# Optimization experiments

Measured on AMD Instinct MI355X. Metric: run time of the kernel, lower is better.

## Reference

```python
import jax, jax.numpy as jnp
import numpy as np

N_NODES = 50000
N_EDGES = 800000
F_IN = 32
F_OUT = 32
NB = 4  # basis terms per dimension


def linear_basis(x, n):
    # Piecewise-linear 'hat' basis on [-1, 1] with n equispaced centers.
    # f_k(x) = max(0, 1 - |x - c_k| / dx),  c_k = linspace(-1, 1, n), dx = 2/(n-1)
    centers = jnp.linspace(-1.0, 1.0, n, dtype=x.dtype)
    dx = 2.0 / (n - 1)
    return jnp.maximum(0.0, 1.0 - jnp.abs(x[:, None] - centers) / dx)  # [E, n]


def setup_inputs() -> dict:
    key = jax.random.key(0)
    k0, k1, k2, k3, k4 = jax.random.split(key, 5)
    x_i = jax.random.normal(k0, (N_NODES, F_IN), dtype=jnp.float32)
    x_j = jax.random.normal(k1, (N_NODES, F_IN), dtype=jnp.float32)
    edge_index = jax.random.randint(k2, (2, N_EDGES), 0, N_NODES)  # row0=target, row1=source
    edge_attr = jax.random.uniform(k3, (N_EDGES, 2), dtype=jnp.float32,
                                   minval=-1.0, maxval=1.0)
    # torch init: uniform_(-0.05, 0.05) on [NB, NB, F_IN, F_OUT]
    weight = jax.random.uniform(k4, (NB, NB, F_IN, F_OUT), dtype=jnp.float32,
                                minval=-0.05, maxval=0.05)
    return {"x_i": x_i, "x_j": x_j, "edge_index": edge_index,
            "edge_attr": edge_attr, "weight": weight}


def reference(x_i, x_j, edge_index, edge_attr, weight):
    dst = edge_index[0]  # aggregation target nodes
    src = edge_index[1]  # source nodes (features gathered from x_j)

    bx = linear_basis(edge_attr[:, 0], NB)            # [E, NB]
    by = linear_basis(edge_attr[:, 1], NB)            # [E, NB]
    b = (bx[:, :, None] * by[:, None, :]).reshape(-1, NB * NB)  # [E, NB*NB]

    feat = x_j[src]                                   # [E, F_IN] edge gather
    w = weight.reshape(NB * NB, F_IN, F_OUT)          # [K, F_IN, F_OUT]
    msg = jnp.einsum('ek,ei,kio->eo', b, feat, w)     # [E, F_OUT]

    # weighted scatter-add to target nodes
    out = jax.ops.segment_sum(msg, dst, num_segments=x_i.shape[0])  # [N, F_OUT]
    return out
```

## Files before the change

kernel.cpp:

```cpp
#include <hip/hip_runtime.h>
#include <hip/hip_bf16.h>

typedef short short8 __attribute__((ext_vector_type(8)));
typedef float f32x4 __attribute__((ext_vector_type(4)));
typedef unsigned uint4v __attribute__((ext_vector_type(4)));

#define F 32
#define NB 4
#define BINSH 5
#define BINSZ 32
#define EPB 512
#define SCH 4096
#define MAXBIN 2048
#define CAPB 2048
#define OSCH 2048
#define OMAXNBLK 1024

__device__ __forceinline__ short f2bf(float f) {
    unsigned u = __float_as_uint(f);
    unsigned r = (u + 0x7FFFu + ((u >> 16) & 1u)) >> 16;
    return (short)r;
}

__device__ __forceinline__ unsigned pk2(float a, float b) {
    __hip_bfloat162 h = __float22bfloat162_rn(make_float2(a, b));
    union { __hip_bfloat162 h; unsigned u; } cv; cv.h = h; return cv.u;
}

__global__ __launch_bounds__(256) void w_prep(
    const float* __restrict__ w, short* __restrict__ wbf)
{
    int idx = blockIdx.x * 256 + threadIdx.x;
    int k = idx >> 10, rem = idx & 1023, i = rem >> 5, o = rem & 31;
    int slot = (((k * 4 + (i >> 3)) * 2 + (o >> 4)) * 16 + (o & 15)) * 8 + (i & 7);
    wbf[slot] = f2bf(w[idx]);
}

__global__ __launch_bounds__(256) void h2_kernel(
    const int* __restrict__ ei, const float* __restrict__ attr, int E, int nbin,
    int* __restrict__ bincnt, int* __restrict__ cellcnt)
{
    __shared__ int hb[MAXBIN];
    __shared__ int hc[9];
    int t = threadIdx.x;
    for (int i = t; i < nbin; i += 256) hb[i] = 0;
    if (t < 9) hc[t] = 0;
    __syncthreads();
    int stride = gridDim.x * blockDim.x;
    for (int e = blockIdx.x * blockDim.x + t; e < E; e += stride) {
        int dst = ei[e];
        float2 a = reinterpret_cast<const float2*>(attr)[e];
        float tx = fminf(fmaxf((a.x + 1.0f) * 1.5f, 0.f), 3.f);
        float ty = fminf(fmaxf((a.y + 1.0f) * 1.5f, 0.f), 3.f);
        int kx = min((int)tx, 2), ky = min((int)ty, 2);
        atomicAdd(&hb[dst >> BINSH], 1);
        atomicAdd(&hc[kx * 3 + ky], 1);
    }
    __syncthreads();
    for (int i = t; i < nbin; i += 256)
        if (hb[i]) atomicAdd(&bincnt[i], hb[i]);
    if (t < 9 && hc[t]) atomicAdd(&cellcnt[t], hc[t]);
}

__global__ __launch_bounds__(256) void scan2_kernel(
    const int* __restrict__ bincnt, int* __restrict__ binbase,
    int* __restrict__ bincur, const int* __restrict__ cellcnt,
    int* __restrict__ cellbase, int* __restrict__ cellcur,
    int* __restrict__ blkoff, int nbin)
{
    __shared__ int part[256];
    int t = threadIdx.x;
    int chunk = (nbin + 255) / 256;
    int lo = t * chunk, hi = min(lo + chunk, nbin);
    int s = 0;
    for (int q = lo; q < hi; ++q) s += bincnt[q];
    part[t] = s;
    __syncthreads();
    if (t == 0) {
        int run = 0;
        for (int j = 0; j < 256; ++j) { int v = part[j]; part[j] = run; run += v; }
        binbase[nbin] = run;
    }
    __syncthreads();
    int run = part[t];
    for (int q = lo; q < hi; ++q) {
        binbase[q] = run; bincur[q] = run;
        run += bincnt[q];
    }
    if (t == 0) {
        int off = 0, boff = 0;
        for (int c = 0; c < 9; ++c) {
            cellbase[c] = off; cellcur[c] = off; blkoff[c] = boff;
            off  += cellcnt[c];
            boff += (cellcnt[c] + EPB - 1) / EPB;
        }
        cellbase[9] = off; blkoff[9] = boff;
    }
}

__global__ __launch_bounds__(256) void scat2_kernel(
    const int* __restrict__ ei, const float* __restrict__ attr, int E, int nbin,
    int* __restrict__ bincur, int* __restrict__ cellcur,
    uint4* __restrict__ cellrec, unsigned char* __restrict__ dloc8)
{
    __shared__ int hb[MAXBIN];
    __shared__ int hc[9];
    int t = threadIdx.x, b = blockIdx.x;
    int start = b * SCH, end = min(start + SCH, E);
    for (int i = t; i < nbin; i += 256) hb[i] = 0;
    if (t < 9) hc[t] = 0;
    __syncthreads();
    for (int e = start + t; e < end; e += 256) {
        int dst = ei[e];
        float2 a = reinterpret_cast<const float2*>(attr)[e];
        float tx = fminf(fmaxf((a.x + 1.0f) * 1.5f, 0.f), 3.f);
        float ty = fminf(fmaxf((a.y + 1.0f) * 1.5f, 0.f), 3.f);
        int kx = min((int)tx, 2), ky = min((int)ty, 2);
        atomicAdd(&hb[dst >> BINSH], 1);
        atomicAdd(&hc[kx * 3 + ky], 1);
    }
    __syncthreads();
    for (int k = t; k < nbin; k += 256) {
        int c = hb[k];
        if (c) hb[k] = atomicAdd(&bincur[k], c);
    }
    if (t < 9) hc[t] = atomicAdd(&cellcur[t], hc[t]);
    __syncthreads();
    for (int e = start + t; e < end; e += 256) {
        int dst = ei[e];
        int src = ei[E + e];
        float2 a = reinterpret_cast<const float2*>(attr)[e];
        float tx = fminf(fmaxf((a.x + 1.0f) * 1.5f, 0.f), 3.f);
        float ty = fminf(fmaxf((a.y + 1.0f) * 1.5f, 0.f), 3.f);
        int kx = min((int)tx, 2), ky = min((int)ty, 2);
        int pd = atomicAdd(&hb[dst >> BINSH], 1);
        int pc = atomicAdd(&hc[kx * 3 + ky], 1);
        uint4 rec;
        rec.x = (unsigned)src;
        rec.y = (unsigned)pd;
        rec.z = __float_as_uint(tx);
        rec.w = __float_as_uint(ty);
        cellrec[pc] = rec;
        dloc8[pd] = (unsigned char)(dst & (BINSZ - 1));
    }
}

__global__ __launch_bounds__(256, 4) void bconv_msg(
    const float* __restrict__ x_j, const short* __restrict__ wbf,
    const int* __restrict__ cellbase, const int* __restrict__ blkoff,
    const uint4* __restrict__ cellrec, unsigned* __restrict__ msg)
{
    int b = blockIdx.x;
    if (b >= blkoff[9]) return;
    int c = 0;
    #pragma unroll
    for (int q = 1; q < 9; ++q) c += (b >= blkoff[q]) ? 1 : 0;
    int kx0 = c / 3, ky0 = c - 3 * (c / 3);
    int local  = b - blkoff[c];
    int cstart = cellbase[c], cend = cellbase[c + 1];
    int pstart = cstart + local * EPB;
    int pend   = min(pstart + EPB, cend);
    if (pstart >= pend) return;

    int t = threadIdx.x;
    int wid = t >> 6, lane = t & 63;
    int row16 = lane & 15, hi = lane >> 4;

    short8 w0[4], w1[4];
    #pragma unroll
    for (int kk = 0; kk < 4; ++kk) {
        int ks = (kx0 + (kk >> 1)) * NB + (ky0 + (kk & 1));
        w0[kk] = *reinterpret_cast<const short8*>(
            wbf + (((ks * 4 + hi) * 2 + 0) * 16 + row16) * 8);
        w1[kk] = *reinterpret_cast<const short8*>(
            wbf + (((ks * 4 + hi) * 2 + 1) * 16 + row16) * 8);
    }

    const float4* x4 = reinterpret_cast<const float4*>(x_j);
    int ntile = (pend - pstart + 15) >> 4;

    auto fetch = [&](int ti, uint4& rec, float4& fa, float4& fb, int& pdv) {
        int p = pstart + ti * 16 + row16;
        bool v = p < pend;
        int pp = v ? p : pstart;
        rec = cellrec[pp];
        int src = rec.x;
        fa = x4[src * 8 + 2 * hi];
        fb = x4[src * 8 + 2 * hi + 1];
        pdv = v ? (int)rec.y : -1;
    };

    int it = wid;
    uint4 rec; float4 fa, fb; int pdv;
    if (it < ntile) fetch(it, rec, fa, fb, pdv);

    for (; it < ntile; it += 4) {
        uint4 recN; float4 faN, fbN; int pdvN = -1;
        bool hn = (it + 4) < ntile;
        if (hn) fetch(it + 4, recN, faN, fbN, pdvN);

        float tx = __uint_as_float(rec.z), ty = __uint_as_float(rec.w);
        float fx = tx - (float)kx0, fy = ty - (float)ky0;
        float bx0 = 1.f - fx, by0 = 1.f - fy;
        float bc[4] = { bx0 * by0, bx0 * fy, fx * by0, fx * fy };
        float fl[8] = { fa.x, fa.y, fa.z, fa.w, fb.x, fb.y, fb.z, fb.w };

        f32x4 a0 = {0,0,0,0}, a1 = {0,0,0,0};
        #pragma unroll
        for (int kk = 0; kk < 4; ++kk) {
            float s = bc[kk];
            uint4v u;
            u[0] = pk2(fl[0] * s, fl[1] * s);
            u[1] = pk2(fl[2] * s, fl[3] * s);
            u[2] = pk2(fl[4] * s, fl[5] * s);
            u[3] = pk2(fl[6] * s, fl[7] * s);
            short8 av = __builtin_bit_cast(short8, u);
            a0 = __builtin_amdgcn_mfma_f32_16x16x32_bf16(av, w0[kk], a0, 0, 0, 0);
            a1 = __builtin_amdgcn_mfma_f32_16x16x32_bf16(av, w1[kk], a1, 0, 0, 0);
        }
        #pragma unroll
        for (int r = 0; r < 4; ++r) {
            int pd = __shfl(pdv, 4 * hi + r, 64);
            if (pd >= 0)
                msg[(size_t)pd * 16 + row16] = pk2(a0[r], a1[r]);
        }
        rec = recN; fa = faN; fb = fbN; pdv = pdvN;
    }
}

__global__ __launch_bounds__(256, 8) void bconv_reduce(
    const unsigned* __restrict__ msg, const unsigned char* __restrict__ dloc8,
    const int* __restrict__ binbase, float* __restrict__ out, int N)
{
    __shared__ unsigned short perm[CAPB];
    __shared__ int cnt[32], cbase[33], cur[32];

    int t = threadIdx.x, bin = blockIdx.x;
    int g = t >> 3, j = t & 7;
    int s0 = binbase[bin], s1 = binbase[bin + 1];
    const uint2* m2 = reinterpret_cast<const uint2*>(msg);

    float aAlo = 0.f, aAhi = 0.f, aBlo = 0.f, aBhi = 0.f;

    for (int chunk = s0; chunk < s1; chunk += CAPB) {
        int clen = min(CAPB, s1 - chunk);
        if (t < 32) cnt[t] = 0;
        __syncthreads();
        for (int i = t; i < clen; i += 256)
            atomicAdd(&cnt[dloc8[chunk + i]], 1);
        __syncthreads();
        if (t == 0) {
            int run = 0;
            #pragma unroll
            for (int c2 = 0; c2 < 32; ++c2) { cbase[c2] = run; run += cnt[c2]; }
            cbase[32] = run;
        }
        __syncthreads();
        if (t < 32) cur[t] = cbase[t];
        __syncthreads();
        for (int i = t; i < clen; i += 256) {
            int d = dloc8[chunk + i];
            int r = atomicAdd(&cur[d], 1);
            perm[r] = (unsigned short)i;
        }
        __syncthreads();

        int lo = cbase[g], hi2 = cbase[g + 1];
        int k = lo;
        for (; k + 3 < hi2; k += 4) {
            int i0 = perm[k], i1 = perm[k + 1], i2 = perm[k + 2], i3 = perm[k + 3];
            uint2 v0 = m2[(size_t)(chunk + i0) * 8 + j];
            uint2 v1 = m2[(size_t)(chunk + i1) * 8 + j];
            uint2 v2 = m2[(size_t)(chunk + i2) * 8 + j];
            uint2 v3 = m2[(size_t)(chunk + i3) * 8 + j];
            aAlo += __uint_as_float(v0.x << 16); aAhi += __uint_as_float(v0.x & 0xFFFF0000u);
            aBlo += __uint_as_float(v0.y << 16); aBhi += __uint_as_float(v0.y & 0xFFFF0000u);
            aAlo += __uint_as_float(v1.x << 16); aAhi += __uint_as_float(v1.x & 0xFFFF0000u);
            aBlo += __uint_as_float(v1.y << 16); aBhi += __uint_as_float(v1.y & 0xFFFF0000u);
            aAlo += __uint_as_float(v2.x << 16); aAhi += __uint_as_float(v2.x & 0xFFFF0000u);
            aBlo += __uint_as_float(v2.y << 16); aBhi += __uint_as_float(v2.y & 0xFFFF0000u);
            aAlo += __uint_as_float(v3.x << 16); aAhi += __uint_as_float(v3.x & 0xFFFF0000u);
            aBlo += __uint_as_float(v3.y << 16); aBhi += __uint_as_float(v3.y & 0xFFFF0000u);
        }
        for (; k < hi2; ++k) {
            int i0 = perm[k];
            uint2 v0 = m2[(size_t)(chunk + i0) * 8 + j];
            aAlo += __uint_as_float(v0.x << 16); aAhi += __uint_as_float(v0.x & 0xFFFF0000u);
            aBlo += __uint_as_float(v0.y << 16); aBhi += __uint_as_float(v0.y & 0xFFFF0000u);
        }
        __syncthreads();
    }

    int node = bin * BINSZ + g;
    if (node < N) {
        float2 lo2; lo2.x = aAlo; lo2.y = aBlo;
        float2 hi2v; hi2v.x = aAhi; hi2v.y = aBhi;
        *reinterpret_cast<float2*>(&out[(size_t)node * F + 2 * j])      = lo2;
        *reinterpret_cast<float2*>(&out[(size_t)node * F + 16 + 2 * j]) = hi2v;
    }
}

__global__ __launch_bounds__(256) void hist_kernel(
    const float* __restrict__ attr, int E, int* __restrict__ counts)
{
    __shared__ int hh[9];
    int b = blockIdx.x, t = threadIdx.x;
    if (t < 9) hh[t] = 0;
    __syncthreads();
    int start = b * OSCH, end = min(start + OSCH, E);
    for (int e = start + t; e < end; e += 256) {
        float2 a = reinterpret_cast<const float2*>(attr)[e];
        float tx = fminf(fmaxf((a.x + 1.0f) * 1.5f, 0.f), 3.f);
        float ty = fminf(fmaxf((a.y + 1.0f) * 1.5f, 0.f), 3.f);
        atomicAdd(&hh[min((int)tx, 2) * 3 + min((int)ty, 2)], 1);
    }
    __syncthreads();
    if (t < 9) counts[b * 9 + t] = hh[t];
}

__global__ __launch_bounds__(512) void scan_kernel(
    int* __restrict__ ws, int* __restrict__ counts, int nblk)
{
    __shared__ int s[OMAXNBLK * 9];
    __shared__ int tot[9];
    __shared__ int coff[9];
    int n = nblk * 9;
    for (int i = threadIdx.x; i < n; i += 512) s[i] = counts[i];
    __syncthreads();
    if (threadIdx.x < 9) {
        int c = threadIdx.x, run = 0;
        for (int b = 0; b < nblk; ++b) {
            int v = s[b * 9 + c];
            s[b * 9 + c] = run;
            run += v;
        }
        tot[c] = run;
    }
    __syncthreads();
    if (threadIdx.x == 0) {
        int off = 0, boff = 0;
        for (int c = 0; c < 9; ++c) {
            ws[c] = off;  coff[c] = off;
            ws[16 + c] = boff;
            off  += tot[c];
            boff += (tot[c] + EPB - 1) / EPB;
        }
        ws[9] = off;
        ws[16 + 9] = boff;
    }
    __syncthreads();
    for (int i = threadIdx.x; i < n; i += 512)
        counts[i] = s[i] + coff[i % 9];
}

__global__ __launch_bounds__(256) void scatter_kernel(
    const float* __restrict__ attr, int E,
    const int* __restrict__ bases, int* __restrict__ sorted)
{
    __shared__ int cur[9];
    int b = blockIdx.x, t = threadIdx.x;
    if (t < 9) cur[t] = bases[b * 9 + t];
    __syncthreads();
    int start = b * OSCH, end = min(start + OSCH, E);
    for (int e = start + t; e < end; e += 256) {
        float2 a = reinterpret_cast<const float2*>(attr)[e];
        float tx = fminf(fmaxf((a.x + 1.0f) * 1.5f, 0.f), 3.f);
        float ty = fminf(fmaxf((a.y + 1.0f) * 1.5f, 0.f), 3.f);
        int c = min((int)tx, 2) * 3 + min((int)ty, 2);
        int pos = atomicAdd(&cur[c], 1);
        sorted[pos] = e;
    }
}

__global__ __launch_bounds__(256) void bconv_mfma(
    const float* __restrict__ x_j, const int* __restrict__ ei,
    const float* __restrict__ attr, const float* __restrict__ weight,
    const int* __restrict__ ws, const int* __restrict__ sorted,
    float* __restrict__ out, int E)
{
    int b = blockIdx.x;
    const int* blkoff = ws + 16;
    if (b >= blkoff[9]) return;
    int c = 0;
    #pragma unroll
    for (int q = 1; q < 9; ++q) c += (b >= blkoff[q]) ? 1 : 0;
    int kx0 = c / 3, ky0 = c - 3 * (c / 3);
    int local  = b - blkoff[c];
    int cstart = ws[c], cend = ws[c + 1];
    int pstart = cstart + local * EPB;
    int pend   = min(pstart + EPB, cend);

    int t = threadIdx.x;
    int wid = t >> 6, lane = t & 63;
    int row16 = lane & 15, hi = lane >> 4;

    short8 wb[4][2];
    #pragma unroll
    for (int kk = 0; kk < 4; ++kk) {
        int ks = (kx0 + (kk >> 1)) * NB + (ky0 + (kk & 1));
        const float* wp = weight + (size_t)ks * F * F;
        #pragma unroll
        for (int n = 0; n < 2; ++n) {
            short8 v;
            #pragma unroll
            for (int j = 0; j < 8; ++j)
                v[j] = f2bf(wp[(8 * hi + j) * F + row16 + 16 * n]);
            wb[kk][n] = v;
        }
    }

    int wstart = pstart + wid * (EPB / 4);
    int wend   = min(wstart + (EPB / 4), pend);
    if (wstart >= wend) return;

    int ntiles = (wend - wstart + 15) >> 4;
    for (int tt = 0; tt < ntiles; ++tt) {
        int p = wstart + tt * 16 + row16;
        bool v = p < wend;
        int pp = v ? p : wstart;
        int e  = sorted[pp];
        int dst = ei[e];
        int srcn = ei[E + e];
        float2 a = reinterpret_cast<const float2*>(attr)[e];
        const float4* xr = reinterpret_cast<const float4*>(x_j + (size_t)srcn * F);
        float4 fa = xr[2 * hi];
        float4 fb = xr[2 * hi + 1];

        float fx = (a.x + 1.0f) * 1.5f - (float)kx0;
        float fy = (a.y + 1.0f) * 1.5f - (float)ky0;
        float vs = v ? 1.f : 0.f;
        float bx0 = (1.f - fx) * vs, bx1 = fx * vs;
        float bc[4] = { bx0 * (1.f - fy), bx0 * fy, bx1 * (1.f - fy), bx1 * fy };

        f32x4 a0 = {0,0,0,0}, a1 = {0,0,0,0};
        #pragma unroll
        for (int kk = 0; kk < 4; ++kk) {
            float s = bc[kk];
            uint4v u;
            u[0] = pk2(fa.x * s, fa.y * s);
            u[1] = pk2(fa.z * s, fa.w * s);
            u[2] = pk2(fb.x * s, fb.y * s);
            u[3] = pk2(fb.z * s, fb.w * s);
            short8 av = __builtin_bit_cast(short8, u);
            a0 = __builtin_amdgcn_mfma_f32_16x16x32_bf16(av, wb[kk][0], a0, 0, 0, 0);
            a1 = __builtin_amdgcn_mfma_f32_16x16x32_bf16(av, wb[kk][1], a1, 0, 0, 0);
        }
        #pragma unroll
        for (int r = 0; r < 4; ++r) {
            int d = __shfl(v ? dst : -1, 4 * hi + r, 64);
            if (d >= 0) {
                atomicAdd(&out[(size_t)d * F + row16],      a0[r]);
                atomicAdd(&out[(size_t)d * F + 16 + row16], a1[r]);
            }
        }
    }
}

__global__ __launch_bounds__(256) void bconv_fallback(
    const float* __restrict__ x_j, const int* __restrict__ ei,
    const float* __restrict__ attr, const float* __restrict__ weight,
    float* __restrict__ out, int E)
{
    __shared__ float wl[16 * F * F];
    __shared__ float featl[8][F];
    for (int idx = threadIdx.x; idx < 4096; idx += 256)
        reinterpret_cast<float4*>(wl)[idx] = reinterpret_cast<const float4*>(weight)[idx];
    __syncthreads();

    int lane = threadIdx.x & 31, eslot = threadIdx.x >> 5;
    for (int p = blockIdx.x * 8 + eslot; p < E; p += gridDim.x * 8) {
        int dst = ei[p], srcn = ei[E + p];
        float ax = attr[2 * p], ay = attr[2 * p + 1];
        featl[eslot][lane] = x_j[(size_t)srcn * F + lane];
        float tx = (ax + 1.0f) * 1.5f, ty = (ay + 1.0f) * 1.5f;
        int kx0 = min(max((int)tx, 0), 2), ky0 = min(max((int)ty, 0), 2);
        float fx = tx - kx0, fy = ty - ky0;
        float bcv[4] = { (1.0f - fx) * (1.0f - fy), (1.0f - fx) * fy,
                         fx * (1.0f - fy), fx * fy };
        float msg = 0.f;
        const float4* f4 = reinterpret_cast<const float4*>(&featl[eslot][0]);
        #pragma unroll
        for (int kk = 0; kk < 4; ++kk) {
            int k = (kx0 + (kk >> 1)) * NB + (ky0 + (kk & 1));
            const float* wk = wl + k * F * F;
            float a2 = 0.f;
            #pragma unroll
            for (int j = 0; j < 8; ++j) {
                float4 f = f4[j];
                a2 = fmaf(f.x, wk[(4 * j + 0) * F + lane], a2);
                a2 = fmaf(f.y, wk[(4 * j + 1) * F + lane], a2);
                a2 = fmaf(f.z, wk[(4 * j + 2) * F + lane], a2);
                a2 = fmaf(f.w, wk[(4 * j + 3) * F + lane], a2);
            }
            msg = fmaf(bcv[kk], a2, msg);
        }
        atomicAdd(&out[(size_t)dst * F + lane], msg);
    }
}

extern "C" void kernel_launch(void* const* d_in, const int* in_sizes, int n_in,
                              void* d_out, int out_size, void* d_ws, size_t ws_size,
                              hipStream_t stream) {
    const float* x_j    = (const float*)d_in[1];
    const int*   ei     = (const int*)d_in[2];
    const float* attr   = (const float*)d_in[3];
    const float* weight = (const float*)d_in[4];
    float* out = (float*)d_out;
    int E = in_sizes[2] / 2;
    int N = in_sizes[0] / F;

    int nbin = (N + BINSZ - 1) >> BINSH;

    int o_bincnt   = 0;
    int o_cellcnt  = o_bincnt + nbin;
    int o_binbase  = o_cellcnt + 9;
    int o_bincur   = o_binbase + nbin + 1;
    int o_cellbase = o_bincur + nbin;
    int o_cellcur  = o_cellbase + 10;
    int o_blkoff   = o_cellcur + 9;
    int o_wbf      = (o_blkoff + 10 + 3) & ~3;
    int o_dloc     = o_wbf + 8192;
    int o_cellrec  = (o_dloc + (E + 3) / 4 + 3) & ~3;
    size_t o_msg   = (size_t)((o_cellrec + 4 * (size_t)E + 3) & ~3);
    size_t need_new = (o_msg + 16 * (size_t)E) * sizeof(int);

    int nblk_sort = (E + OSCH - 1) / OSCH;
    int sorted_off = 32 + ((nblk_sort * 9 + 15) & ~15);
    size_t need_old = (size_t)(sorted_off + E) * sizeof(int);

    if (nbin <= MAXBIN && N <= 65536 && E < (1 << 24) && ws_size >= need_new) {
        int* ws = (int*)d_ws;
        short* wbf = (short*)(ws + o_wbf);
        unsigned char* dloc8 = (unsigned char*)(ws + o_dloc);
        uint4* cellrec = (uint4*)(ws + o_cellrec);
        unsigned* msg = (unsigned*)(ws + o_msg);

        hipMemsetAsync(ws, 0, (size_t)(nbin + 9) * sizeof(int), stream);
        w_prep<<<64, 256, 0, stream>>>(weight, wbf);
        h2_kernel<<<256, 256, 0, stream>>>(ei, attr, E, nbin,
                                           ws + o_bincnt, ws + o_cellcnt);
        scan2_kernel<<<1, 256, 0, stream>>>(ws + o_bincnt, ws + o_binbase,
                                            ws + o_bincur, ws + o_cellcnt,
                                            ws + o_cellbase, ws + o_cellcur,
                                            ws + o_blkoff, nbin);
        scat2_kernel<<<(E + SCH - 1) / SCH, 256, 0, stream>>>(
            ei, attr, E, nbin, ws + o_bincur, ws + o_cellcur, cellrec, dloc8);
        int nblkA = (E + EPB - 1) / EPB + 9;
        bconv_msg<<<nblkA, 256, 0, stream>>>(x_j, wbf, ws + o_cellbase,
                                             ws + o_blkoff, cellrec, msg);
        bconv_reduce<<<nbin, 256, 0, stream>>>(msg, dloc8, ws + o_binbase, out, N);
    } else if (nblk_sort <= OMAXNBLK && ws_size >= need_old) {
        hipMemsetAsync(d_out, 0, (size_t)out_size * sizeof(float), stream);
        int* ws      = (int*)d_ws;
        int* counts  = ws + 32;
        int* sorted  = ws + sorted_off;
        hist_kernel<<<nblk_sort, 256, 0, stream>>>(attr, E, counts);
        scan_kernel<<<1, 512, 0, stream>>>(ws, counts, nblk_sort);
        scatter_kernel<<<nblk_sort, 256, 0, stream>>>(attr, E, counts, sorted);
        int nblk_main = (E + EPB - 1) / EPB + 9;
        bconv_mfma<<<nblk_main, 256, 0, stream>>>(x_j, ei, attr, weight, ws, sorted, out, E);
    } else {
        hipMemsetAsync(d_out, 0, (size_t)out_size * sizeof(float), stream);
        bconv_fallback<<<2048, 256, 0, stream>>>(x_j, ei, attr, weight, out, E);
    }
}
```

Measured before the change: 98.70 us.

## Sort edges by combined cell-and-destination-bin key with compact packed records

Replaces the separate destination-bin and cell sorts with one counting sort keyed on (cell, dst bin). Per-block histograms are written out, summed, scanned and turned into per-block bases, so the scatter needs no global atomics. Edge records shrink from 16 to 8 bytes by packing the 16-bit source index with 16-bit quantized coordinates. Messages are stored in sorted order, so the message writes become contiguous and the reduce walks nine key segments per bin. This adds more kernel launches and a large shared histogram (about 57 KB), and the 16-bit coordinate quantization loses some precision.

```diff
diff --git a/kernel.cpp b/kernel.cpp
--- a/kernel.cpp
+++ b/kernel.cpp
@@ -10,9 +10,11 @@
 #define BINSH 5
 #define BINSZ 32
 #define EPB 512
-#define SCH 4096
-#define MAXBIN 2048
 #define CAPB 2048
+#define SCH2 8192
+#define MAXBIN2 1600
+#define NKEYMAX (9 * MAXBIN2)
+#define NBLK2MAX 128
 #define OSCH 2048
 #define OMAXNBLK 1024
 
@@ -36,119 +38,122 @@
     wbf[slot] = f2bf(w[idx]);
 }
 
-__global__ __launch_bounds__(256) void h2_kernel(
-    const int* __restrict__ ei, const float* __restrict__ attr, int E, int nbin,
-    int* __restrict__ bincnt, int* __restrict__ cellcnt)
-{
-    __shared__ int hb[MAXBIN];
-    __shared__ int hc[9];
-    int t = threadIdx.x;
-    for (int i = t; i < nbin; i += 256) hb[i] = 0;
-    if (t < 9) hc[t] = 0;
-    __syncthreads();
-    int stride = gridDim.x * blockDim.x;
-    for (int e = blockIdx.x * blockDim.x + t; e < E; e += stride) {
-        int dst = ei[e];
-        float2 a = reinterpret_cast<const float2*>(attr)[e];
-        float tx = fminf(fmaxf((a.x + 1.0f) * 1.5f, 0.f), 3.f);
-        float ty = fminf(fmaxf((a.y + 1.0f) * 1.5f, 0.f), 3.f);
-        int kx = min((int)tx, 2), ky = min((int)ty, 2);
-        atomicAdd(&hb[dst >> BINSH], 1);
-        atomicAdd(&hc[kx * 3 + ky], 1);
-    }
-    __syncthreads();
-    for (int i = t; i < nbin; i += 256)
-        if (hb[i]) atomicAdd(&bincnt[i], hb[i]);
-    if (t < 9 && hc[t]) atomicAdd(&cellcnt[t], hc[t]);
-}
-
-__global__ __launch_bounds__(256) void scan2_kernel(
-    const int* __restrict__ bincnt, int* __restrict__ binbase,
-    int* __restrict__ bincur, const int* __restrict__ cellcnt,
-    int* __restrict__ cellbase, int* __restrict__ cellcur,
-    int* __restrict__ blkoff, int nbin)
-{
-    __shared__ int part[256];
-    int t = threadIdx.x;
-    int chunk = (nbin + 255) / 256;
-    int lo = t * chunk, hi = min(lo + chunk, nbin);
-    int s = 0;
-    for (int q = lo; q < hi; ++q) s += bincnt[q];
-    part[t] = s;
-    __syncthreads();
-    if (t == 0) {
-        int run = 0;
-        for (int j = 0; j < 256; ++j) { int v = part[j]; part[j] = run; run += v; }
-        binbase[nbin] = run;
-    }
-    __syncthreads();
-    int run = part[t];
-    for (int q = lo; q < hi; ++q) {
-        binbase[q] = run; bincur[q] = run;
-        run += bincnt[q];
-    }
-    if (t == 0) {
-        int off = 0, boff = 0;
-        for (int c = 0; c < 9; ++c) {
-            cellbase[c] = off; cellcur[c] = off; blkoff[c] = boff;
-            off  += cellcnt[c];
-            boff += (cellcnt[c] + EPB - 1) / EPB;
-        }
-        cellbase[9] = off; blkoff[9] = boff;
-    }
-}
-
-__global__ __launch_bounds__(256) void scat2_kernel(
-    const int* __restrict__ ei, const float* __restrict__ attr, int E, int nbin,
-    int* __restrict__ bincur, int* __restrict__ cellcur,
-    uint4* __restrict__ cellrec, unsigned char* __restrict__ dloc8)
-{
-    __shared__ int hb[MAXBIN];
-    __shared__ int hc[9];
+
+__global__ __launch_bounds__(256) void k1_hist(
+    const int* __restrict__ ei, const float* __restrict__ attr, int E,
+    int nbin, int nkey, int* __restrict__ counts)
+{
+    __shared__ int h[NKEYMAX];
     int t = threadIdx.x, b = blockIdx.x;
-    int start = b * SCH, end = min(start + SCH, E);
-    for (int i = t; i < nbin; i += 256) hb[i] = 0;
-    if (t < 9) hc[t] = 0;
-    __syncthreads();
+    for (int i = t; i < nkey; i += 256) h[i] = 0;
+    __syncthreads();
+    int start = b * SCH2, end = min(start + SCH2, E);
     for (int e = start + t; e < end; e += 256) {
         int dst = ei[e];
         float2 a = reinterpret_cast<const float2*>(attr)[e];
         float tx = fminf(fmaxf((a.x + 1.0f) * 1.5f, 0.f), 3.f);
         float ty = fminf(fmaxf((a.y + 1.0f) * 1.5f, 0.f), 3.f);
         int kx = min((int)tx, 2), ky = min((int)ty, 2);
-        atomicAdd(&hb[dst >> BINSH], 1);
-        atomicAdd(&hc[kx * 3 + ky], 1);
-    }
-    __syncthreads();
-    for (int k = t; k < nbin; k += 256) {
-        int c = hb[k];
-        if (c) hb[k] = atomicAdd(&bincur[k], c);
-    }
-    if (t < 9) hc[t] = atomicAdd(&cellcur[t], hc[t]);
-    __syncthreads();
+        atomicAdd(&h[(kx * 3 + ky) * nbin + (dst >> BINSH)], 1);
+    }
+    __syncthreads();
+    int* d = counts + (size_t)b * nkey;
+    for (int i = t; i < nkey; i += 256) d[i] = h[i];
+}
+
+__global__ __launch_bounds__(256) void k2a_tot(
+    const int* __restrict__ counts, int* __restrict__ keytot,
+    int nkey, int nblk)
+{
+    int k = blockIdx.x * 256 + threadIdx.x;
+    if (k >= nkey) return;
+    int s = 0;
+    for (int b = 0; b < nblk; ++b) s += counts[(size_t)b * nkey + k];
+    keytot[k] = s;
+}
+
+__global__ __launch_bounds__(256) void k2b_scan(
+    const int* __restrict__ keytot, int* __restrict__ keybase,
+    int* __restrict__ blkoff, int nkey, int nbin, int Etot)
+{
+    __shared__ int part[256];
+    int t = threadIdx.x;
+    int chunk = (nkey + 255) / 256;
+    int lo = t * chunk, hi = min(lo + chunk, nkey);
+    int s = 0;
+    for (int q = lo; q < hi; ++q) s += keytot[q];
+    part[t] = s;
+    __syncthreads();
+    if (t == 0) {
+        int run = 0;
+        for (int j = 0; j < 256; ++j) { int v = part[j]; part[j] = run; run += v; }
+        keybase[nkey] = Etot;
+    }
+    __syncthreads();
+    int run = part[t];
+    for (int q = lo; q < hi; ++q) { keybase[q] = run; run += keytot[q]; }
+    __syncthreads();
+    if (t == 0) {
+        int boff = 0;
+        for (int c = 0; c < 9; ++c) {
+            blkoff[c] = boff;
+            int cs = keybase[c * nbin];
+            int ce = keybase[(c + 1) * nbin];
+            boff += (ce - cs + EPB - 1) / EPB;
+        }
+        blkoff[9] = boff;
+    }
+}
+
+__global__ __launch_bounds__(256) void k2c_base(
+    int* __restrict__ counts, const int* __restrict__ keybase,
+    int nkey, int nblk)
+{
+    int k = blockIdx.x * 256 + threadIdx.x;
+    if (k >= nkey) return;
+    int run = keybase[k];
+    for (int b = 0; b < nblk; ++b) {
+        size_t idx = (size_t)b * nkey + k;
+        int v = counts[idx];
+        counts[idx] = run;
+        run += v;
+    }
+}
+
+__global__ __launch_bounds__(256) void k3_scat(
+    const int* __restrict__ ei, const float* __restrict__ attr, int E,
+    int nbin, int nkey, const int* __restrict__ counts,
+    uint2* __restrict__ rec, unsigned char* __restrict__ dloc8)
+{
+    __shared__ int cur[NKEYMAX];
+    int t = threadIdx.x, b = blockIdx.x;
+    const int* base = counts + (size_t)b * nkey;
+    for (int i = t; i < nkey; i += 256) cur[i] = base[i];
+    __syncthreads();
+    int start = b * SCH2, end = min(start + SCH2, E);
     for (int e = start + t; e < end; e += 256) {
         int dst = ei[e];
-        int src = ei[E + e];
+        int sn  = ei[E + e];
         float2 a = reinterpret_cast<const float2*>(attr)[e];
         float tx = fminf(fmaxf((a.x + 1.0f) * 1.5f, 0.f), 3.f);
         float ty = fminf(fmaxf((a.y + 1.0f) * 1.5f, 0.f), 3.f);
         int kx = min((int)tx, 2), ky = min((int)ty, 2);
-        int pd = atomicAdd(&hb[dst >> BINSH], 1);
-        int pc = atomicAdd(&hc[kx * 3 + ky], 1);
-        uint4 rec;
-        rec.x = (unsigned)src;
-        rec.y = (unsigned)pd;
-        rec.z = __float_as_uint(tx);
-        rec.w = __float_as_uint(ty);
-        cellrec[pc] = rec;
-        dloc8[pd] = (unsigned char)(dst & (BINSZ - 1));
-    }
-}
-
-__global__ __launch_bounds__(256, 4) void bconv_msg(
+        int k = (kx * 3 + ky) * nbin + (dst >> BINSH);
+        int pos = atomicAdd(&cur[k], 1);
+        unsigned txq = (unsigned)(tx * 21845.0f + 0.5f);
+        unsigned tyq = (unsigned)(ty * 21845.0f + 0.5f);
+        uint2 r;
+        r.x = (unsigned)sn | (txq << 16);
+        r.y = tyq | ((unsigned)(dst & (BINSZ - 1)) << 16);
+        rec[pos] = r;
+        dloc8[pos] = (unsigned char)(dst & (BINSZ - 1));
+    }
+}
+
+__global__ __launch_bounds__(256, 4) void bconv_msgS(
     const float* __restrict__ x_j, const short* __restrict__ wbf,
-    const int* __restrict__ cellbase, const int* __restrict__ blkoff,
-    const uint4* __restrict__ cellrec, unsigned* __restrict__ msg)
+    const int* __restrict__ keybase, const int* __restrict__ blkoff,
+    const uint2* __restrict__ rec, unsigned* __restrict__ msg, int nbin)
 {
     int b = blockIdx.x;
     if (b >= blkoff[9]) return;
@@ -157,7 +162,8 @@
     for (int q = 1; q < 9; ++q) c += (b >= blkoff[q]) ? 1 : 0;
     int kx0 = c / 3, ky0 = c - 3 * (c / 3);
     int local  = b - blkoff[c];
-    int cstart = cellbase[c], cend = cellbase[c + 1];
+    int cstart = keybase[c * nbin];
+    int cend   = keybase[(c + 1) * nbin];
     int pstart = cstart + local * EPB;
     int pend   = min(pstart + EPB, cend);
     if (pstart >= pend) return;
@@ -179,27 +185,26 @@
     const float4* x4 = reinterpret_cast<const float4*>(x_j);
     int ntile = (pend - pstart + 15) >> 4;
 
-    auto fetch = [&](int ti, uint4& rec, float4& fa, float4& fb, int& pdv) {
+    auto fetch = [&](int ti, uint2& r2, float4& fa, float4& fb) {
         int p = pstart + ti * 16 + row16;
-        bool v = p < pend;
-        int pp = v ? p : pstart;
-        rec = cellrec[pp];
-        int src = rec.x;
-        fa = x4[src * 8 + 2 * hi];
-        fb = x4[src * 8 + 2 * hi + 1];
-        pdv = v ? (int)rec.y : -1;
+        int pp = min(p, pend - 1);
+        r2 = rec[pp];
+        int sn = r2.x & 0xFFFF;
+        fa = x4[sn * 8 + 2 * hi];
+        fb = x4[sn * 8 + 2 * hi + 1];
     };
 
     int it = wid;
-    uint4 rec; float4 fa, fb; int pdv;
-    if (it < ntile) fetch(it, rec, fa, fb, pdv);
+    uint2 r2; float4 fa, fb;
+    if (it < ntile) fetch(it, r2, fa, fb);
 
     for (; it < ntile; it += 4) {
-        uint4 recN; float4 faN, fbN; int pdvN = -1;
+        uint2 r2N; float4 faN, fbN;
         bool hn = (it + 4) < ntile;
-        if (hn) fetch(it + 4, recN, faN, fbN, pdvN);
-
-        float tx = __uint_as_float(rec.z), ty = __uint_as_float(rec.w);
+        if (hn) fetch(it + 4, r2N, faN, fbN);
+
+        float tx = (float)(r2.x >> 16)     * (1.f / 21845.f);
+        float ty = (float)(r2.y & 0xFFFF)  * (1.f / 21845.f);
         float fx = tx - (float)kx0, fy = ty - (float)ky0;
         float bx0 = 1.f - fx, by0 = 1.f - fy;
         float bc[4] = { bx0 * by0, bx0 * fy, fx * by0, fx * fy };
@@ -218,77 +223,81 @@
             a0 = __builtin_amdgcn_mfma_f32_16x16x32_bf16(av, w0[kk], a0, 0, 0, 0);
             a1 = __builtin_amdgcn_mfma_f32_16x16x32_bf16(av, w1[kk], a1, 0, 0, 0);
         }
+        int tb = pstart + it * 16;
         #pragma unroll
         for (int r = 0; r < 4; ++r) {
-            int pd = __shfl(pdv, 4 * hi + r, 64);
-            if (pd >= 0)
-                msg[(size_t)pd * 16 + row16] = pk2(a0[r], a1[r]);
-        }
-        rec = recN; fa = faN; fb = fbN; pdv = pdvN;
-    }
-}
-
-__global__ __launch_bounds__(256, 8) void bconv_reduce(
+            int row = tb + 4 * hi + r;
+            if (row < pend)
+                msg[(size_t)row * 16 + row16] = pk2(a0[r], a1[r]);
+        }
+        r2 = r2N; fa = faN; fb = fbN;
+    }
+}
+
+__global__ __launch_bounds__(256, 8) void bconv_reduceS(
     const unsigned* __restrict__ msg, const unsigned char* __restrict__ dloc8,
-    const int* __restrict__ binbase, float* __restrict__ out, int N)
+    const int* __restrict__ keybase, int nbin, float* __restrict__ out, int N)
 {
     __shared__ unsigned short perm[CAPB];
     __shared__ int cnt[32], cbase[33], cur[32];
 
     int t = threadIdx.x, bin = blockIdx.x;
     int g = t >> 3, j = t & 7;
-    int s0 = binbase[bin], s1 = binbase[bin + 1];
     const uint2* m2 = reinterpret_cast<const uint2*>(msg);
 
     float aAlo = 0.f, aAhi = 0.f, aBlo = 0.f, aBhi = 0.f;
 
-    for (int chunk = s0; chunk < s1; chunk += CAPB) {
-        int clen = min(CAPB, s1 - chunk);
-        if (t < 32) cnt[t] = 0;
-        __syncthreads();
-        for (int i = t; i < clen; i += 256)
-            atomicAdd(&cnt[dloc8[chunk + i]], 1);
-        __syncthreads();
-        if (t == 0) {
-            int run = 0;
-            #pragma unroll
-            for (int c2 = 0; c2 < 32; ++c2) { cbase[c2] = run; run += cnt[c2]; }
-            cbase[32] = run;
-        }
-        __syncthreads();
-        if (t < 32) cur[t] = cbase[t];
-        __syncthreads();
-        for (int i = t; i < clen; i += 256) {
-            int d = dloc8[chunk + i];
-            int r = atomicAdd(&cur[d], 1);
-            perm[r] = (unsigned short)i;
-        }
-        __syncthreads();
-
-        int lo = cbase[g], hi2 = cbase[g + 1];
-        int k = lo;
-        for (; k + 3 < hi2; k += 4) {
-            int i0 = perm[k], i1 = perm[k + 1], i2 = perm[k + 2], i3 = perm[k + 3];
-            uint2 v0 = m2[(size_t)(chunk + i0) * 8 + j];
-            uint2 v1 = m2[(size_t)(chunk + i1) * 8 + j];
-            uint2 v2 = m2[(size_t)(chunk + i2) * 8 + j];
-            uint2 v3 = m2[(size_t)(chunk + i3) * 8 + j];
-            aAlo += __uint_as_float(v0.x << 16); aAhi += __uint_as_float(v0.x & 0xFFFF0000u);
-            aBlo += __uint_as_float(v0.y << 16); aBhi += __uint_as_float(v0.y & 0xFFFF0000u);
-            aAlo += __uint_as_float(v1.x << 16); aAhi += __uint_as_float(v1.x & 0xFFFF0000u);
-            aBlo += __uint_as_float(v1.y << 16); aBhi += __uint_as_float(v1.y & 0xFFFF0000u);
-            aAlo += __uint_as_float(v2.x << 16); aAhi += __uint_as_float(v2.x & 0xFFFF0000u);
-            aBlo += __uint_as_float(v2.y << 16); aBhi += __uint_as_float(v2.y & 0xFFFF0000u);
-            aAlo += __uint_as_float(v3.x << 16); aAhi += __uint_as_float(v3.x & 0xFFFF0000u);
-            aBlo += __uint_as_float(v3.y << 16); aBhi += __uint_as_float(v3.y & 0xFFFF0000u);
-        }
-        for (; k < hi2; ++k) {
-            int i0 = perm[k];
-            uint2 v0 = m2[(size_t)(chunk + i0) * 8 + j];
-            aAlo += __uint_as_float(v0.x << 16); aAhi += __uint_as_float(v0.x & 0xFFFF0000u);
-            aBlo += __uint_as_float(v0.y << 16); aBhi += __uint_as_float(v0.y & 0xFFFF0000u);
-        }
-        __syncthreads();
+    for (int c = 0; c < 9; ++c) {
+        int k = c * nbin + bin;
+        int s0 = keybase[k], s1 = keybase[k + 1];
+        for (int chunk = s0; chunk < s1; chunk += CAPB) {
+            int clen = min(CAPB, s1 - chunk);
+            if (t < 32) cnt[t] = 0;
+            __syncthreads();
+            for (int i = t; i < clen; i += 256)
+                atomicAdd(&cnt[dloc8[chunk + i]], 1);
+            __syncthreads();
+            if (t == 0) {
+                int run = 0;
+                #pragma unroll
+                for (int c2 = 0; c2 < 32; ++c2) { cbase[c2] = run; run += cnt[c2]; }
+                cbase[32] = run;
+            }
+            __syncthreads();
+            if (t < 32) cur[t] = cbase[t];
+            __syncthreads();
+            for (int i = t; i < clen; i += 256) {
+                int d = dloc8[chunk + i];
+                int r = atomicAdd(&cur[d], 1);
+                perm[r] = (unsigned short)i;
+            }
+            __syncthreads();
+
+            int lo = cbase[g], hi2 = cbase[g + 1];
+            int kk = lo;
+            for (; kk + 3 < hi2; kk += 4) {
+                int i0 = perm[kk], i1 = perm[kk + 1], i2 = perm[kk + 2], i3 = perm[kk + 3];
+                uint2 v0 = m2[(size_t)(chunk + i0) * 8 + j];
+                uint2 v1 = m2[(size_t)(chunk + i1) * 8 + j];
+                uint2 v2 = m2[(size_t)(chunk + i2) * 8 + j];
+                uint2 v3 = m2[(size_t)(chunk + i3) * 8 + j];
+                aAlo += __uint_as_float(v0.x << 16); aAhi += __uint_as_float(v0.x & 0xFFFF0000u);
+                aBlo += __uint_as_float(v0.y << 16); aBhi += __uint_as_float(v0.y & 0xFFFF0000u);
+                aAlo += __uint_as_float(v1.x << 16); aAhi += __uint_as_float(v1.x & 0xFFFF0000u);
+                aBlo += __uint_as_float(v1.y << 16); aBhi += __uint_as_float(v1.y & 0xFFFF0000u);
+                aAlo += __uint_as_float(v2.x << 16); aAhi += __uint_as_float(v2.x & 0xFFFF0000u);
+                aBlo += __uint_as_float(v2.y << 16); aBhi += __uint_as_float(v2.y & 0xFFFF0000u);
+                aAlo += __uint_as_float(v3.x << 16); aAhi += __uint_as_float(v3.x & 0xFFFF0000u);
+                aBlo += __uint_as_float(v3.y << 16); aBhi += __uint_as_float(v3.y & 0xFFFF0000u);
+            }
+            for (; kk < hi2; ++kk) {
+                int i0 = perm[kk];
+                uint2 v0 = m2[(size_t)(chunk + i0) * 8 + j];
+                aAlo += __uint_as_float(v0.x << 16); aAhi += __uint_as_float(v0.x & 0xFFFF0000u);
+                aBlo += __uint_as_float(v0.y << 16); aBhi += __uint_as_float(v0.y & 0xFFFF0000u);
+            }
+            __syncthreads();
+        }
     }
 
     int node = bin * BINSZ + g;
@@ -357,9 +366,9 @@
     const float* __restrict__ attr, int E,
     const int* __restrict__ bases, int* __restrict__ sorted)
 {
-    __shared__ int cur[9];
+    __shared__ int cur9[9];
     int b = blockIdx.x, t = threadIdx.x;
-    if (t < 9) cur[t] = bases[b * 9 + t];
+    if (t < 9) cur9[t] = bases[b * 9 + t];
     __syncthreads();
     int start = b * OSCH, end = min(start + OSCH, E);
     for (int e = start + t; e < end; e += 256) {
@@ -367,7 +376,7 @@
         float tx = fminf(fmaxf((a.x + 1.0f) * 1.5f, 0.f), 3.f);
         float ty = fminf(fmaxf((a.y + 1.0f) * 1.5f, 0.f), 3.f);
         int c = min((int)tx, 2) * 3 + min((int)ty, 2);
-        int pos = atomicAdd(&cur[c], 1);
+        int pos = atomicAdd(&cur9[c], 1);
         sorted[pos] = e;
     }
 }
@@ -510,45 +519,45 @@
     int N = in_sizes[0] / F;
 
     int nbin = (N + BINSZ - 1) >> BINSH;
-
-    int o_bincnt   = 0;
-    int o_cellcnt  = o_bincnt + nbin;
-    int o_binbase  = o_cellcnt + 9;
-    int o_bincur   = o_binbase + nbin + 1;
-    int o_cellbase = o_bincur + nbin;
-    int o_cellcur  = o_cellbase + 10;
-    int o_blkoff   = o_cellcur + 9;
-    int o_wbf      = (o_blkoff + 10 + 3) & ~3;
-    int o_dloc     = o_wbf + 8192;
-    int o_cellrec  = (o_dloc + (E + 3) / 4 + 3) & ~3;
-    size_t o_msg   = (size_t)((o_cellrec + 4 * (size_t)E + 3) & ~3);
-    size_t need_new = (o_msg + 16 * (size_t)E) * sizeof(int);
+    int nkey = 9 * nbin;
+    int nblk2 = (E + SCH2 - 1) / SCH2;
+
+    size_t o_counts  = 0;
+    size_t o_keytot  = o_counts + (size_t)nblk2 * nkey;
+    size_t o_keybase = o_keytot + nkey;
+    size_t o_blkoff  = o_keybase + nkey + 1;
+    size_t o_wbf     = (o_blkoff + 10 + 3) & ~(size_t)3;
+    size_t o_dloc    = o_wbf + 8192;
+    size_t o_rec     = (o_dloc + (E + 3) / 4 + 1) & ~(size_t)1;
+    size_t o_msg     = (o_rec + 2 * (size_t)E + 3) & ~(size_t)3;
+    size_t need_new  = (o_msg + 16 * (size_t)E) * sizeof(int);
 
     int nblk_sort = (E + OSCH - 1) / OSCH;
     int sorted_off = 32 + ((nblk_sort * 9 + 15) & ~15);
     size_t need_old = (size_t)(sorted_off + E) * sizeof(int);
 
-    if (nbin <= MAXBIN && N <= 65536 && E < (1 << 24) && ws_size >= need_new) {
+    if (nbin <= MAXBIN2 && N <= MAXBIN2 * BINSZ && nblk2 <= NBLK2MAX &&
+        ws_size >= need_new) {
         int* ws = (int*)d_ws;
-        short* wbf = (short*)(ws + o_wbf);
+        int* counts   = ws + o_counts;
+        int* keytot   = ws + o_keytot;
+        int* keybase  = ws + o_keybase;
+        int* blkoff   = ws + o_blkoff;
+        short* wbf    = (short*)(ws + o_wbf);
         unsigned char* dloc8 = (unsigned char*)(ws + o_dloc);
-        uint4* cellrec = (uint4*)(ws + o_cellrec);
+        uint2* rec    = (uint2*)(ws + o_rec);
         unsigned* msg = (unsigned*)(ws + o_msg);
 
-        hipMemsetAsync(ws, 0, (size_t)(nbin + 9) * sizeof(int), stream);
+        int nkb = (nkey + 255) / 256;
         w_prep<<<64, 256, 0, stream>>>(weight, wbf);
-        h2_kernel<<<256, 256, 0, stream>>>(ei, attr, E, nbin,
-                                           ws + o_bincnt, ws + o_cellcnt);
-        scan2_kernel<<<1, 256, 0, stream>>>(ws + o_bincnt, ws + o_binbase,
-                                            ws + o_bincur, ws + o_cellcnt,
-                                            ws + o_cellbase, ws + o_cellcur,
-                                            ws + o_blkoff, nbin);
-        scat2_kernel<<<(E + SCH - 1) / SCH, 256, 0, stream>>>(
-            ei, attr, E, nbin, ws + o_bincur, ws + o_cellcur, cellrec, dloc8);
+        k1_hist<<<nblk2, 256, 0, stream>>>(ei, attr, E, nbin, nkey, counts);
+        k2a_tot<<<nkb, 256, 0, stream>>>(counts, keytot, nkey, nblk2);
+        k2b_scan<<<1, 256, 0, stream>>>(keytot, keybase, blkoff, nkey, nbin, E);
+        k2c_base<<<nkb, 256, 0, stream>>>(counts, keybase, nkey, nblk2);
+        k3_scat<<<nblk2, 256, 0, stream>>>(ei, attr, E, nbin, nkey, counts, rec, dloc8);
         int nblkA = (E + EPB - 1) / EPB + 9;
-        bconv_msg<<<nblkA, 256, 0, stream>>>(x_j, wbf, ws + o_cellbase,
-                                             ws + o_blkoff, cellrec, msg);
-        bconv_reduce<<<nbin, 256, 0, stream>>>(msg, dloc8, ws + o_binbase, out, N);
+        bconv_msgS<<<nblkA, 256, 0, stream>>>(x_j, wbf, keybase, blkoff, rec, msg, nbin);
+        bconv_reduceS<<<nbin, 256, 0, stream>>>(msg, dloc8, keybase, nbin, out, N);
     } else if (nblk_sort <= OMAXNBLK && ws_size >= need_old) {
         hipMemsetAsync(d_out, 0, (size_t)out_size * sizeof(float), stream);
         int* ws      = (int*)d_ws;
```

New measurement: 170.6 us. +72.8%, slower.
